# Kernel tuning notes

Measured on AMD Instinct MI355X. Metric: run time of the kernel, lower is better.

Reference implementation:

```python
import jax, jax.numpy as jnp
import numpy as np

D_MODEL = 1024
NUM_HEADS = 16
D_K = D_MODEL // NUM_HEADS
S, B = 2048, 2


def setup_inputs() -> dict:
    key = jax.random.key(0)
    ks = jax.random.split(key, 11)
    lim = 1.0 / np.sqrt(D_MODEL)
    def lin(kw, kb):
        W = jax.random.uniform(kw, (D_MODEL, D_MODEL), jnp.float32, -lim, lim)
        b = jax.random.uniform(kb, (D_MODEL,), jnp.float32, -lim, lim)
        return W, b
    Wq, bq = lin(ks[0], ks[1])
    Wk, bk = lin(ks[2], ks[3])
    Wv, bv = lin(ks[4], ks[5])
    Wo, bo = lin(ks[6], ks[7])
    q = jax.random.normal(ks[8], (S, B, D_MODEL), jnp.float32)
    k = jax.random.normal(ks[9], (S, B, D_MODEL), jnp.float32)
    v = jax.random.normal(ks[10], (S, B, D_MODEL), jnp.float32)
    return {"q": q, "k": k, "v": v,
            "Wq": Wq, "bq": bq, "Wk": Wk, "bk": bk,
            "Wv": Wv, "bv": bv, "Wo": Wo, "bo": bo}


def reference(q, k, v, Wq, bq, Wk, bk, Wv, bv, Wo, bo):
    s, b, _ = q.shape
    scale = np.sqrt(D_K).astype(np.float32)
    # torch Linear: x @ W.T + b
    def proj(x, W, bias):
        y = jnp.einsum('sbd,ed->sbe', x, W) + bias
        # [S,B,D] -> [B,H,S,d_k]
        return y.reshape(s, b, NUM_HEADS, D_K).transpose(1, 2, 0, 3)
    Q = proj(q, Wq, bq)
    K = proj(k, Wk, bk)
    V = proj(v, Wv, bv)
    scores = jnp.einsum('bhsd,bhtd->bhst', Q, K) / scale  # [B,H,S,S]
    attn = jax.nn.softmax(scores, axis=-1)
    ctx = jnp.einsum('bhst,bhtd->bhsd', attn, V)  # [B,H,S,d_k]
    ctx = ctx.transpose(2, 0, 1, 3).reshape(s, b, NUM_HEADS * D_K)
    return jnp.einsum('sbd,ed->sbe', ctx, Wo) + bo
```

## Files before the change

kernel.cpp:

```cpp
#include <hip/hip_runtime.h>
#include <stdint.h>

typedef __attribute__((ext_vector_type(8))) short short8;
typedef __attribute__((ext_vector_type(4))) float f32x4;
typedef __attribute__((ext_vector_type(16))) float f32x16;

#define MFMA16(a, b, c) __builtin_amdgcn_mfma_f32_16x16x32_bf16((a), (b), (c), 0, 0, 0)
#define MFMA32(a, b, c) __builtin_amdgcn_mfma_f32_32x32x16_bf16((a), (b), (c), 0, 0, 0)

__device__ inline unsigned short f2bf(float x) {
  unsigned u = __float_as_uint(x);
  u = (u + 0x7FFFu + ((u >> 16) & 1u)) >> 16;
  return (unsigned short)u;
}

__device__ inline void gload16(const unsigned short* g, unsigned short* l) {
  __builtin_amdgcn_global_load_lds(
      (const __attribute__((address_space(1))) unsigned int*)g,
      (__attribute__((address_space(3))) unsigned int*)l, 16, 0, 0);
}

__device__ inline short8 lds8(const unsigned short* base, int byteoff) {
  return *reinterpret_cast<const short8*>(reinterpret_cast<const char*>(base) + byteoff);
}

__device__ inline unsigned cvtpk(float lo, float hi) {
  unsigned r;
  asm("v_cvt_pk_bf16_f32 %0, %1, %2" : "=v"(r) : "v"(lo), "v"(hi));
  return r;
}
__device__ inline void plswap(unsigned& a, unsigned& b) {
  asm volatile("v_permlane32_swap_b32 %0, %1" : "+v"(a), "+v"(b));
}

__device__ inline short8 mk8(unsigned a, unsigned b, unsigned c, unsigned d) {
  union { unsigned u[4]; short8 v; } x;
  x.u[0] = a; x.u[1] = b; x.u[2] = c; x.u[3] = d;
  return x.v;
}

__device__ inline int swz(int row, int chunk) {
  return row * 128 + (((chunk) ^ (row & 7)) << 4);
}

__global__ __launch_bounds__(256) void cvt_bf16x(const float* __restrict__ a0,
                                                 const float* __restrict__ a1,
                                                 const float* __restrict__ a2,
                                                 const float* __restrict__ a3,
                                                 unsigned short* __restrict__ d, int per) {
  int y = blockIdx.y;
  const float* s = (y == 0) ? a0 : (y == 1) ? a1 : (y == 2) ? a2 : a3;
  int i = (blockIdx.x * 256 + threadIdx.x) * 8;
  if (i >= per) return;
  float4 v0 = *reinterpret_cast<const float4*>(s + i);
  float4 v1 = *reinterpret_cast<const float4*>(s + i + 4);
  short8 o;
  o[0] = (short)f2bf(v0.x); o[1] = (short)f2bf(v0.y);
  o[2] = (short)f2bf(v0.z); o[3] = (short)f2bf(v0.w);
  o[4] = (short)f2bf(v1.x); o[5] = (short)f2bf(v1.y);
  o[6] = (short)f2bf(v1.z); o[7] = (short)f2bf(v1.w);
  *reinterpret_cast<short8*>(d + (size_t)y * per + i) = o;
}

template <int MODE>
__global__ __launch_bounds__(256) void gemm_bt(
    const unsigned short* __restrict__ Abase, const unsigned short* __restrict__ Wbase,
    const float* __restrict__ bias0, const float* __restrict__ bias1,
    const float* __restrict__ bias2, unsigned short* __restrict__ ObaseBf,
    float* __restrict__ ObaseF, int M, int N, int K) {
  constexpr int CHUNK = (MODE == 0) ? 192 : 64;

  const int orig = blockIdx.x;
  const int wg = (orig & 7) * CHUNK + (orig >> 3);
  int z, bx, by;
  if (MODE == 0) {
    z = wg >> 9;
    int r = wg & 511;
    by = r & 15;
    bx = r >> 4;
  } else {
    z = 0; by = wg & 15; bx = wg >> 4;
  }

  const unsigned short* A = Abase + (size_t)z * M * K;
  const unsigned short* W = Wbase + (size_t)z * N * K;
  const float* bias = (z == 0) ? bias0 : (z == 1 ? bias1 : bias2);

  __shared__ unsigned short As[2 * 128 * 64];
  __shared__ unsigned short Bs[2 * 64 * 64];

  const int t = threadIdx.x;
  const int lane = t & 63, w = t >> 6;
  const int wm = w >> 1, wn = w & 1;
  const int m0 = bx * 128, n0 = by * 64;
  const int lrow = lane & 15, lg = lane >> 4;

  f32x4 acc[4][2] = {};

  int arow[4], acol[4], brow[2], bcol[2];
#pragma unroll
  for (int p = 0; p < 4; ++p) {
    int c = (p * 4 + w) * 64 + lane;
    arow[p] = c >> 3; acol[p] = ((c & 7) ^ (arow[p] & 7)) * 8;
  }
#pragma unroll
  for (int p = 0; p < 2; ++p) {
    int c = (p * 4 + w) * 64 + lane;
    brow[p] = c >> 3; bcol[p] = ((c & 7) ^ (brow[p] & 7)) * 8;
  }

#define STAGE_G(kt, buf)                                                              \
  {                                                                                   \
    _Pragma("unroll") for (int p = 0; p < 4; ++p)                                     \
        gload16(&A[(size_t)(m0 + arow[p]) * K + (kt) + acol[p]],                      \
                &As[(buf)*8192 + ((p * 4 + w) * 64) * 8]);                            \
    _Pragma("unroll") for (int p = 0; p < 2; ++p)                                     \
        gload16(&W[(size_t)(n0 + brow[p]) * K + (kt) + bcol[p]],                      \
                &Bs[(buf)*4096 + ((p * 4 + w) * 64) * 8]);                            \
  }

#define COMPUTE(buf)                                                                  \
  {                                                                                   \
    _Pragma("unroll") for (int kc = 0; kc < 2; ++kc) {                                \
      short8 af[4], bfr[2];                                                           \
      _Pragma("unroll") for (int i = 0; i < 4; ++i)                                   \
          af[i] = lds8(As, (buf)*16384 + swz(wm * 64 + i * 16 + lrow, kc * 4 + lg));  \
      _Pragma("unroll") for (int i = 0; i < 2; ++i)                                   \
          bfr[i] = lds8(Bs, (buf)*8192 + swz(wn * 32 + i * 16 + lrow, kc * 4 + lg));  \
      _Pragma("unroll") for (int mi = 0; mi < 4; ++mi)                                \
          _Pragma("unroll") for (int ni = 0; ni < 2; ++ni)                            \
              acc[mi][ni] = MFMA16(af[mi], bfr[ni], acc[mi][ni]);                     \
    }                                                                                 \
  }

  STAGE_G(0, 0);
  asm volatile("s_waitcnt vmcnt(0)" ::: "memory");
  __builtin_amdgcn_s_barrier();
  __builtin_amdgcn_sched_barrier(0);

  int cur = 0;
  for (int kt = 0; kt < K - 64; kt += 64) {
    STAGE_G(kt + 64, cur ^ 1);
    COMPUTE(cur);
    asm volatile("s_waitcnt vmcnt(0)" ::: "memory");
    __builtin_amdgcn_s_barrier();
    __builtin_amdgcn_sched_barrier(0);
    cur ^= 1;
  }
  COMPUTE(cur);
#undef STAGE_G
#undef COMPUTE

  const int r0 = lg * 4;
  if (MODE == 0) {
    const float scale = (z == 0) ? 0.18033688011112042f : 1.0f;
    if (z < 2) {
      unsigned short* O = ObaseBf + (size_t)z * (size_t)M * N;
#pragma unroll
      for (int mi = 0; mi < 4; ++mi)
#pragma unroll
        for (int ni = 0; ni < 2; ++ni) {
          int e = n0 + wn * 32 + ni * 16 + lrow;
          float be = bias[e];
          int h = e >> 6, d = e & 63;
#pragma unroll
          for (int r = 0; r < 4; ++r) {
            int m = m0 + wm * 64 + mi * 16 + r0 + r;
            int s = m >> 1, bb = m & 1;
            O[(((size_t)(bb * 16 + h) * 2048 + s) << 6) + d] = f2bf((acc[mi][ni][r] + be) * scale);
          }
        }
    } else {
      unsigned short* O = ObaseBf + (size_t)2 * (size_t)M * N;
#pragma unroll
      for (int mi = 0; mi < 4; ++mi)
#pragma unroll
        for (int ni = 0; ni < 2; ++ni) {
          int e = n0 + wn * 32 + ni * 16 + lrow;
          float be = bias[e];
          int h = e >> 6, d = e & 63;
#pragma unroll
          for (int r = 0; r < 4; ++r) {
            int m = m0 + wm * 64 + mi * 16 + r0 + r;
            int s = m >> 1, bb = m & 1;
            O[(((size_t)(bb * 16 + h) * 64 + d) << 11) + s] = f2bf(acc[mi][ni][r] + be);
          }
        }
    }
  } else {
    float* O = ObaseF;
#pragma unroll
    for (int mi = 0; mi < 4; ++mi)
#pragma unroll
      for (int ni = 0; ni < 2; ++ni) {
        int e = n0 + wn * 32 + ni * 16 + lrow;
        float be = bias[e];
#pragma unroll
        for (int r = 0; r < 4; ++r) {
          int m = m0 + wm * 64 + mi * 16 + r0 + r;
          O[(size_t)m * N + e] = acc[mi][ni][r] + be;
        }
      }
  }
}

__global__ __launch_bounds__(256) void attn(const unsigned short* __restrict__ Q,
                                            const unsigned short* __restrict__ K,
                                            const unsigned short* __restrict__ Vt,
                                            unsigned short* __restrict__ ctx) {
  __shared__ unsigned short Ks[4 * 4096];
  __shared__ unsigned short Vs[4 * 4096];

  const int orig = blockIdx.x;
  const int wg = ((orig & 7) << 6) + (orig >> 3);
  const int bh = wg >> 4;
  const int qb = wg & 15;

  const int t = threadIdx.x, lane = t & 63, wv = t >> 6;
  const int q0 = qb * 128 + wv * 32;
  const int q = lane & 31, hi = lane >> 5;
  const int fq = (q ^ (q >> 3)) & 7;

  const unsigned short* Qb = Q + ((size_t)bh * 2048 + q0) * 64;
  const unsigned short* Kb = K + (size_t)bh * 2048 * 64;
  const unsigned short* Vb = Vt + (size_t)bh * 64 * 2048;

  short8 qf[4];
#pragma unroll
  for (int m = 0; m < 4; ++m)
    qf[m] = *reinterpret_cast<const short8*>(&Qb[q * 64 + m * 16 + hi * 8]);

  const short8 ones = {0x3F80, 0x3F80, 0x3F80, 0x3F80, 0x3F80, 0x3F80, 0x3F80, 0x3F80};

  int koff[2][4], voff[2][2][2];
#pragma unroll
  for (int st = 0; st < 2; ++st) {
    int f = fq ^ (st ? 4 : 0);
#pragma unroll
    for (int m = 0; m < 4; ++m)
      koff[st][m] = (st * 32 + q) * 128 + (((m * 2 + hi) ^ f) << 4);
  }
#pragma unroll
  for (int dh = 0; dh < 2; ++dh) {
    int f = fq ^ (dh ? 4 : 0);
#pragma unroll
    for (int st = 0; st < 2; ++st)
#pragma unroll
      for (int kc = 0; kc < 2; ++kc)
        voff[dh][st][kc] = (dh * 32 + q) * 128 + (((st * 4 + kc * 2 + hi) ^ f) << 4);
  }

  int c0 = wv * 64 + lane, c1 = (4 + wv) * 64 + lane;
  int sr0 = c0 >> 3, sr1 = c1 >> 3;
  int sc0c = ((c0 & 7) ^ ((sr0 ^ (sr0 >> 3)) & 7)) * 8;
  int sc1c = ((c1 & 7) ^ ((sr1 ^ (sr1 >> 3)) & 7)) * 8;
  const unsigned short* ks0 = Kb + (size_t)sr0 * 64 + sc0c;
  const unsigned short* ks1 = Kb + (size_t)sr1 * 64 + sc1c;
  const unsigned short* vp0 = Vb + (size_t)sr0 * 2048 + sc0c;
  const unsigned short* vp1 = Vb + (size_t)sr1 * 2048 + sc1c;

  f32x16 oa0 = {}, oa1 = {}, osum = {};

#pragma unroll
  for (int pt = 0; pt < 3; ++pt) {
    char* kb = (char*)Ks + pt * 8192;
    char* vb2 = (char*)Vs + pt * 8192;
    gload16(ks0, (unsigned short*)(kb + wv * 1024));
    gload16(ks1, (unsigned short*)(kb + (4 + wv) * 1024));
    gload16(vp0, (unsigned short*)(vb2 + wv * 1024));
    gload16(vp1, (unsigned short*)(vb2 + (4 + wv) * 1024));
    ks0 += 4096; ks1 += 4096; vp0 += 64; vp1 += 64;
  }

  for (int tile = 0; tile < 32; ++tile) {
    asm volatile("s_waitcnt vmcnt(8)" ::: "memory");
    __builtin_amdgcn_s_barrier();
    __builtin_amdgcn_sched_barrier(0);

    {
      char* kb = (char*)Ks + ((tile + 3) & 3) * 8192;
      char* vb2 = (char*)Vs + ((tile + 3) & 3) * 8192;
      gload16(ks0, (unsigned short*)(kb + wv * 1024));
      gload16(ks1, (unsigned short*)(kb + (4 + wv) * 1024));
      gload16(vp0, (unsigned short*)(vb2 + wv * 1024));
      gload16(vp1, (unsigned short*)(vb2 + (4 + wv) * 1024));
      ks0 += 4096; ks1 += 4096; vp0 += 64; vp1 += 64;
    }

    const int cur = (tile & 3) * 8192;
    __builtin_amdgcn_s_setprio(1);

    f32x16 s0 = {}, s1 = {};
#pragma unroll
    for (int m = 0; m < 4; ++m) {
      short8 k0 = lds8(Ks, cur + koff[0][m]);
      short8 k1 = lds8(Ks, cur + koff[1][m]);
      s0 = MFMA32(k0, qf[m], s0);
      s1 = MFMA32(k1, qf[m], s1);
    }

#pragma unroll
    for (int st = 0; st < 2; ++st) {
      const f32x16& sv = st ? s1 : s0;
      float p[16];
#pragma unroll
      for (int i = 0; i < 16; ++i) p[i] = __builtin_amdgcn_exp2f(sv[i]);

      unsigned w0 = cvtpk(p[0], p[1]), w1 = cvtpk(p[2], p[3]);
      unsigned w2 = cvtpk(p[4], p[5]), w3 = cvtpk(p[6], p[7]);
      plswap(w0, w2); plswap(w1, w3);
      unsigned w4 = cvtpk(p[8], p[9]), w5 = cvtpk(p[10], p[11]);
      unsigned w6 = cvtpk(p[12], p[13]), w7 = cvtpk(p[14], p[15]);
      plswap(w4, w6); plswap(w5, w7);
      short8 pa0 = mk8(w0, w1, w2, w3);
      short8 pa1 = mk8(w4, w5, w6, w7);

      osum = MFMA32(pa0, ones, osum);
      oa0 = MFMA32(pa0, lds8(Vs, cur + voff[0][st][0]), oa0);
      oa1 = MFMA32(pa0, lds8(Vs, cur + voff[1][st][0]), oa1);
      osum = MFMA32(pa1, ones, osum);
      oa0 = MFMA32(pa1, lds8(Vs, cur + voff[0][st][1]), oa0);
      oa1 = MFMA32(pa1, lds8(Vs, cur + voff[1][st][1]), oa1);
    }
    __builtin_amdgcn_s_setprio(0);
  }

  const int b = bh >> 4, h = bh & 15;
#pragma unroll
  for (int r = 0; r < 16; ++r) {
    int qr = (r & 3) + 8 * (r >> 2) + 4 * hi;
    float li = 1.0f / osum[r];
    size_t base = ((size_t)(q0 + qr) * 2 + b) * 1024 + h * 64 + q;
    ctx[base] = f2bf(oa0[r] * li);
    ctx[base + 32] = f2bf(oa1[r] * li);
  }
}

extern "C" void kernel_launch(void* const* d_in, const int* in_sizes, int n_in, void* d_out,
                              int out_size, void* d_ws, size_t ws_size, hipStream_t stream) {
  const float* q  = (const float*)d_in[0];
  const float* k  = (const float*)d_in[1];
  const float* v  = (const float*)d_in[2];
  const float* Wq = (const float*)d_in[3];
  const float* bq = (const float*)d_in[4];
  const float* Wk = (const float*)d_in[5];
  const float* bk = (const float*)d_in[6];
  const float* Wv = (const float*)d_in[7];
  const float* bv = (const float*)d_in[8];
  const float* Wo = (const float*)d_in[9];
  const float* bo = (const float*)d_in[10];

  const size_t SZ_IN = 4194304;
  const size_t SZ_W  = 1048576;
  unsigned short* ws  = (unsigned short*)d_ws;
  unsigned short* xb  = ws;
  unsigned short* Wb  = xb + 3 * SZ_IN;
  unsigned short* QKV = Wb + 4 * SZ_W;
  unsigned short* ctx = QKV + 3 * SZ_IN;

  cvt_bf16x<<<dim3(SZ_IN / 2048, 3), 256, 0, stream>>>(q, k, v, v, xb, (int)SZ_IN);
  cvt_bf16x<<<dim3(SZ_W / 2048, 4), 256, 0, stream>>>(Wq, Wk, Wv, Wo, Wb, (int)SZ_W);

  gemm_bt<0><<<1536, 256, 0, stream>>>(xb, Wb, bq, bk, bv, QKV, nullptr, 4096, 1024, 1024);
  attn<<<512, 256, 0, stream>>>(QKV, QKV + SZ_IN, QKV + 2 * SZ_IN, ctx);
  gemm_bt<1><<<512, 256, 0, stream>>>(ctx, Wb + 3 * SZ_W, bo, bo, bo, nullptr,
                                      (float*)d_out, 4096, 1024, 1024);
}
```

Before: 128.6 us.

## Software-pipeline QK of next tile with softmax/PV of current tile in attention

Restructures the attention loop so the QK^T MFMAs for tile t+1 are issued before the exp/pack and PV MFMAs of tile t, letting matrix work overlap the transcendental and permute work. Row sums are now accumulated in VALU from fp32 probabilities and combined across half-waves with a permlane swap, replacing the extra MFMA-with-ones per block. It also requests two workgroups per CU through launch bounds. The cost is more live accumulator registers, which could cause spills under the occupancy target, and a row sum taken from fp32 values instead of the bf16-rounded ones used in PV.

After: 124.2 us. 3.4% less time.

```diff
diff --git a/kernel.cpp b/kernel.cpp
--- a/kernel.cpp
+++ b/kernel.cpp
@@ -32,6 +32,11 @@
 __device__ inline void plswap(unsigned& a, unsigned& b) {
   asm volatile("v_permlane32_swap_b32 %0, %1" : "+v"(a), "+v"(b));
 }
+__device__ inline float swapadd(float v) {
+  float a = v, b;
+  asm volatile("v_mov_b32 %1, %0\n\tv_permlane32_swap_b32 %0, %1" : "+v"(a), "=&v"(b));
+  return a + b;
+}
 
 __device__ inline short8 mk8(unsigned a, unsigned b, unsigned c, unsigned d) {
   union { unsigned u[4]; short8 v; } x;
@@ -41,6 +46,28 @@
 
 __device__ inline int swz(int row, int chunk) {
   return row * 128 + (((chunk) ^ (row & 7)) << 4);
+}
+
+__device__ inline void exppack(const f32x16& sv, float& lsum, short8& paLo, short8& paHi) {
+  float p[16];
+#pragma unroll
+  for (int i = 0; i < 16; ++i) p[i] = __builtin_amdgcn_exp2f(sv[i]);
+  float q8[8];
+#pragma unroll
+  for (int i = 0; i < 8; ++i) q8[i] = p[2 * i] + p[2 * i + 1];
+#pragma unroll
+  for (int s2 = 4; s2 > 0; s2 >>= 1)
+#pragma unroll
+    for (int i = 0; i < s2; ++i) q8[i] += q8[i + s2];
+  lsum += q8[0];
+  unsigned w0 = cvtpk(p[0], p[1]), w1 = cvtpk(p[2], p[3]);
+  unsigned w2 = cvtpk(p[4], p[5]), w3 = cvtpk(p[6], p[7]);
+  plswap(w0, w2); plswap(w1, w3);
+  unsigned w4 = cvtpk(p[8], p[9]), w5 = cvtpk(p[10], p[11]);
+  unsigned w6 = cvtpk(p[12], p[13]), w7 = cvtpk(p[14], p[15]);
+  plswap(w4, w6); plswap(w5, w7);
+  paLo = mk8(w0, w1, w2, w3);
+  paHi = mk8(w4, w5, w6, w7);
 }
 
 __global__ __launch_bounds__(256) void cvt_bf16x(const float* __restrict__ a0,
@@ -204,10 +231,10 @@
   }
 }
 
-__global__ __launch_bounds__(256) void attn(const unsigned short* __restrict__ Q,
-                                            const unsigned short* __restrict__ K,
-                                            const unsigned short* __restrict__ Vt,
-                                            unsigned short* __restrict__ ctx) {
+__global__ __launch_bounds__(256, 2) void attn(const unsigned short* __restrict__ Q,
+                                               const unsigned short* __restrict__ K,
+                                               const unsigned short* __restrict__ Vt,
+                                               unsigned short* __restrict__ ctx) {
   __shared__ unsigned short Ks[4 * 4096];
   __shared__ unsigned short Vs[4 * 4096];
 
@@ -229,8 +256,6 @@
 #pragma unroll
   for (int m = 0; m < 4; ++m)
     qf[m] = *reinterpret_cast<const short8*>(&Qb[q * 64 + m * 16 + hi * 8]);
-
-  const short8 ones = {0x3F80, 0x3F80, 0x3F80, 0x3F80, 0x3F80, 0x3F80, 0x3F80, 0x3F80};
 
   int koff[2][4], voff[2][2][2];
 #pragma unroll
@@ -259,77 +284,96 @@
   const unsigned short* vp0 = Vb + (size_t)sr0 * 2048 + sc0c;
   const unsigned short* vp1 = Vb + (size_t)sr1 * 2048 + sc1c;
 
-  f32x16 oa0 = {}, oa1 = {}, osum = {};
-
-#pragma unroll
-  for (int pt = 0; pt < 3; ++pt) {
-    char* kb = (char*)Ks + pt * 8192;
-    char* vb2 = (char*)Vs + pt * 8192;
-    gload16(ks0, (unsigned short*)(kb + wv * 1024));
-    gload16(ks1, (unsigned short*)(kb + (4 + wv) * 1024));
-    gload16(vp0, (unsigned short*)(vb2 + wv * 1024));
-    gload16(vp1, (unsigned short*)(vb2 + (4 + wv) * 1024));
-    ks0 += 4096; ks1 += 4096; vp0 += 64; vp1 += 64;
-  }
-
-  for (int tile = 0; tile < 32; ++tile) {
-    asm volatile("s_waitcnt vmcnt(8)" ::: "memory");
-    __builtin_amdgcn_s_barrier();
-    __builtin_amdgcn_sched_barrier(0);
-
-    {
-      char* kb = (char*)Ks + ((tile + 3) & 3) * 8192;
-      char* vb2 = (char*)Vs + ((tile + 3) & 3) * 8192;
-      gload16(ks0, (unsigned short*)(kb + wv * 1024));
-      gload16(ks1, (unsigned short*)(kb + (4 + wv) * 1024));
-      gload16(vp0, (unsigned short*)(vb2 + wv * 1024));
-      gload16(vp1, (unsigned short*)(vb2 + (4 + wv) * 1024));
-      ks0 += 4096; ks1 += 4096; vp0 += 64; vp1 += 64;
-    }
-
-    const int cur = (tile & 3) * 8192;
-    __builtin_amdgcn_s_setprio(1);
-
-    f32x16 s0 = {}, s1 = {};
-#pragma unroll
-    for (int m = 0; m < 4; ++m) {
-      short8 k0 = lds8(Ks, cur + koff[0][m]);
-      short8 k1 = lds8(Ks, cur + koff[1][m]);
-      s0 = MFMA32(k0, qf[m], s0);
-      s1 = MFMA32(k1, qf[m], s1);
-    }
-
-#pragma unroll
-    for (int st = 0; st < 2; ++st) {
-      const f32x16& sv = st ? s1 : s0;
-      float p[16];
-#pragma unroll
-      for (int i = 0; i < 16; ++i) p[i] = __builtin_amdgcn_exp2f(sv[i]);
-
-      unsigned w0 = cvtpk(p[0], p[1]), w1 = cvtpk(p[2], p[3]);
-      unsigned w2 = cvtpk(p[4], p[5]), w3 = cvtpk(p[6], p[7]);
-      plswap(w0, w2); plswap(w1, w3);
-      unsigned w4 = cvtpk(p[8], p[9]), w5 = cvtpk(p[10], p[11]);
-      unsigned w6 = cvtpk(p[12], p[13]), w7 = cvtpk(p[14], p[15]);
-      plswap(w4, w6); plswap(w5, w7);
-      short8 pa0 = mk8(w0, w1, w2, w3);
-      short8 pa1 = mk8(w4, w5, w6, w7);
-
-      osum = MFMA32(pa0, ones, osum);
-      oa0 = MFMA32(pa0, lds8(Vs, cur + voff[0][st][0]), oa0);
-      oa1 = MFMA32(pa0, lds8(Vs, cur + voff[1][st][0]), oa1);
-      osum = MFMA32(pa1, ones, osum);
-      oa0 = MFMA32(pa1, lds8(Vs, cur + voff[0][st][1]), oa0);
-      oa1 = MFMA32(pa1, lds8(Vs, cur + voff[1][st][1]), oa1);
-    }
-    __builtin_amdgcn_s_setprio(0);
-  }
-
+#define STAGE(tt)                                                      \
+  {                                                                    \
+    char* kb = (char*)Ks + ((tt) & 3) * 8192;                          \
+    char* vb2 = (char*)Vs + ((tt) & 3) * 8192;                         \
+    gload16(ks0, (unsigned short*)(kb + wv * 1024));                   \
+    gload16(ks1, (unsigned short*)(kb + (4 + wv) * 1024));             \
+    gload16(vp0, (unsigned short*)(vb2 + wv * 1024));                  \
+    gload16(vp1, (unsigned short*)(vb2 + (4 + wv) * 1024));            \
+    ks0 += 4096; ks1 += 4096; vp0 += 64; vp1 += 64;                    \
+  }
+
+  f32x16 oa0 = {}, oa1 = {};
+  float lsum = 0.f;
+  const f32x16 zero16 = {};
+  f32x16 sA0 = {}, sA1 = {}, sB0, sB1;
+
+  STAGE(0); STAGE(1); STAGE(2);
+  asm volatile("s_waitcnt vmcnt(8)" ::: "memory");
+  __builtin_amdgcn_s_barrier();
+  __builtin_amdgcn_sched_barrier(0);
+#pragma unroll
+  for (int m = 0; m < 4; ++m) {
+    sA0 = MFMA32(lds8(Ks, koff[0][m]), qf[m], sA0);
+    sA1 = MFMA32(lds8(Ks, koff[1][m]), qf[m], sA1);
+  }
+
+#define PHASE(tcur, sC0, sC1, sN0, sN1)                                         \
+  {                                                                             \
+    asm volatile("s_waitcnt vmcnt(4)" ::: "memory");                            \
+    __builtin_amdgcn_sched_barrier(0);                                          \
+    __builtin_amdgcn_s_barrier();                                               \
+    __builtin_amdgcn_sched_barrier(0);                                          \
+    STAGE((tcur) + 3);                                                          \
+    sN0 = zero16; sN1 = zero16;                                                 \
+    __builtin_amdgcn_s_setprio(1);                                              \
+    {                                                                           \
+      const int so = (((tcur) + 1) & 3) * 8192;                                 \
+      _Pragma("unroll") for (int m = 0; m < 4; ++m) {                           \
+        sN0 = MFMA32(lds8(Ks, so + koff[0][m]), qf[m], sN0);                    \
+        sN1 = MFMA32(lds8(Ks, so + koff[1][m]), qf[m], sN1);                    \
+      }                                                                         \
+    }                                                                           \
+    short8 paL0, paH0, paL1, paH1;                                              \
+    exppack(sC0, lsum, paL0, paH0);                                             \
+    exppack(sC1, lsum, paL1, paH1);                                             \
+    {                                                                           \
+      const int vo = ((tcur) & 3) * 8192;                                       \
+      oa0 = MFMA32(paL0, lds8(Vs, vo + voff[0][0][0]), oa0);                    \
+      oa1 = MFMA32(paL0, lds8(Vs, vo + voff[1][0][0]), oa1);                    \
+      oa0 = MFMA32(paH0, lds8(Vs, vo + voff[0][0][1]), oa0);                    \
+      oa1 = MFMA32(paH0, lds8(Vs, vo + voff[1][0][1]), oa1);                    \
+      oa0 = MFMA32(paL1, lds8(Vs, vo + voff[0][1][0]), oa0);                    \
+      oa1 = MFMA32(paL1, lds8(Vs, vo + voff[1][1][0]), oa1);                    \
+      oa0 = MFMA32(paH1, lds8(Vs, vo + voff[0][1][1]), oa0);                    \
+      oa1 = MFMA32(paH1, lds8(Vs, vo + voff[1][1][1]), oa1);                    \
+    }                                                                           \
+    __builtin_amdgcn_s_setprio(0);                                              \
+  }
+
+  for (int it = 0; it < 15; ++it) {
+    int tc = 2 * it;
+    PHASE(tc, sA0, sA1, sB0, sB1);
+    PHASE(tc + 1, sB0, sB1, sA0, sA1);
+  }
+  PHASE(30, sA0, sA1, sB0, sB1);
+
+  {
+    short8 paL0, paH0, paL1, paH1;
+    exppack(sB0, lsum, paL0, paH0);
+    exppack(sB1, lsum, paL1, paH1);
+    const int vo = 3 * 8192;
+    oa0 = MFMA32(paL0, lds8(Vs, vo + voff[0][0][0]), oa0);
+    oa1 = MFMA32(paL0, lds8(Vs, vo + voff[1][0][0]), oa1);
+    oa0 = MFMA32(paH0, lds8(Vs, vo + voff[0][0][1]), oa0);
+    oa1 = MFMA32(paH0, lds8(Vs, vo + voff[1][0][1]), oa1);
+    oa0 = MFMA32(paL1, lds8(Vs, vo + voff[0][1][0]), oa0);
+    oa1 = MFMA32(paL1, lds8(Vs, vo + voff[1][1][0]), oa1);
+    oa0 = MFMA32(paH1, lds8(Vs, vo + voff[0][1][1]), oa0);
+    oa1 = MFMA32(paH1, lds8(Vs, vo + voff[1][1][1]), oa1);
+  }
+#undef PHASE
+#undef STAGE
+
+  lsum = swapadd(lsum);
+  float linv = 1.0f / lsum;
   const int b = bh >> 4, h = bh & 15;
 #pragma unroll
   for (int r = 0; r < 16; ++r) {
     int qr = (r & 3) + 8 * (r >> 2) + 4 * hi;
-    float li = 1.0f / osum[r];
+    float li = __shfl(linv, qr);
     size_t base = ((size_t)(q0 + qr) * 2 + b) * 1024 + h * 64 + q;
     ctx[base] = f2bf(oa0[r] * li);
     ctx[base + 32] = f2bf(oa1[r] * li);
```
